# Optimization experiments

Hardware: AMD Instinct MI355X
Metric: run time of the kernel (lower is better)

Reference implementation:

```python
import jax, jax.numpy as jnp
import numpy as np


def setup_inputs() -> dict:
    key = jax.random.key(0)
    ks = jax.random.split(key, 8)
    N, T, U = 8, 512, 64
    E, D, J, V = 512, 512, 512, 500
    s = 0.02
    return {
        "encoder_out": jax.random.normal(ks[0], (N, T, E), jnp.float32),
        "decoder_out": jax.random.normal(ks[1], (N, U, D), jnp.float32),
        "W_enc": jax.random.normal(ks[2], (J, E), jnp.float32) * s,
        "b_enc": jnp.zeros((J,), jnp.float32),
        "W_dec": jax.random.normal(ks[3], (J, D), jnp.float32) * s,
        "b_dec": jnp.zeros((J,), jnp.float32),
        "W_out": jax.random.normal(ks[4], (V, J), jnp.float32) * s,
        "b_out": jnp.zeros((V,), jnp.float32),
    }


def reference(encoder_out, decoder_out, W_enc, b_enc, W_dec, b_dec, W_out, b_out):
    # Project encoder [N,T,E]->[N,T,J] and decoder [N,U,D]->[N,U,J]
    enc = jnp.einsum("nte,je->ntj", encoder_out, W_enc) + b_enc
    dec = jnp.einsum("nud,jd->nuj", decoder_out, W_dec) + b_dec
    # Broadcast add over (T,U), tanh, then vocab projection -> [N,T,U,V]
    activations = jnp.tanh(enc[:, :, None, :] + dec[:, None, :, :])
    logits = jnp.einsum("ntuj,vj->ntuv", activations, W_out) + b_out
    return logits
```

## Files before the change

kernel.cpp:

```cpp
#include <hip/hip_runtime.h>
#include <hip/hip_bf16.h>


typedef __attribute__((ext_vector_type(4))) float f32x4;
typedef __attribute__((ext_vector_type(16))) float f32x16;
typedef __attribute__((ext_vector_type(8))) short s16x8;

static __device__ __forceinline__ unsigned short f2bf(float x) {
    union { float f; unsigned u; } v; v.f = x;
    return (unsigned short)((v.u + 0x7FFFu + ((v.u >> 16) & 1u)) >> 16);
}

static __device__ __forceinline__ float fast_tanh(float x) {
    float e = __expf(2.0f * x);
    float r = __builtin_amdgcn_rcpf(e + 1.0f);
    return __builtin_fmaf(-2.0f, r, 1.0f);
}

static __device__ __forceinline__ unsigned swz64(int r, int c) {
    return (unsigned)(r * 64 + ((c ^ ((r >> 1) & 3)) << 4));
}

__global__ __launch_bounds__(256) void proj_gemm(
    const float* __restrict__ A, const float* __restrict__ W,
    const float* __restrict__ b, float* __restrict__ C)
{
    __shared__ unsigned short As[128 * 64];
    __shared__ unsigned short Bs[128 * 64];
    const int mt = blockIdx.x, jt = blockIdx.y;
    const int tid = threadIdx.x;
    const int lane = tid & 63, wid = tid >> 6;
    const int wm = wid >> 1, wn = wid & 1;

    f32x4 acc[4][4];
    const f32x4 zero = {0.f, 0.f, 0.f, 0.f};
    #pragma unroll
    for (int i = 0; i < 4; ++i)
        #pragma unroll
        for (int j = 0; j < 4; ++j) acc[i][j] = zero;

    const int c8 = (tid & 7) * 8;
    const int rbase = tid >> 3;

    for (int kt = 0; kt < 8; ++kt) {
        __syncthreads();
        #pragma unroll
        for (int p = 0; p < 4; ++p) {
            int r = p * 32 + rbase;
            int byte = (r * 128 + c8 * 2) ^ ((r & 7) << 4);
            {
                const float* s = A + (size_t)(mt * 128 + r) * 512 + kt * 64 + c8;
                f32x4 v0 = *(const f32x4*)s, v1 = *(const f32x4*)(s + 4);
                s16x8 pk;
                pk[0] = (short)f2bf(v0[0]); pk[1] = (short)f2bf(v0[1]);
                pk[2] = (short)f2bf(v0[2]); pk[3] = (short)f2bf(v0[3]);
                pk[4] = (short)f2bf(v1[0]); pk[5] = (short)f2bf(v1[1]);
                pk[6] = (short)f2bf(v1[2]); pk[7] = (short)f2bf(v1[3]);
                *(s16x8*)((char*)As + byte) = pk;
            }
            {
                const float* s = W + (size_t)(jt * 128 + r) * 512 + kt * 64 + c8;
                f32x4 v0 = *(const f32x4*)s, v1 = *(const f32x4*)(s + 4);
                s16x8 pk;
                pk[0] = (short)f2bf(v0[0]); pk[1] = (short)f2bf(v0[1]);
                pk[2] = (short)f2bf(v0[2]); pk[3] = (short)f2bf(v0[3]);
                pk[4] = (short)f2bf(v1[0]); pk[5] = (short)f2bf(v1[1]);
                pk[6] = (short)f2bf(v1[2]); pk[7] = (short)f2bf(v1[3]);
                *(s16x8*)((char*)Bs + byte) = pk;
            }
        }
        __syncthreads();
        #pragma unroll
        for (int kk = 0; kk < 2; ++kk) {
            s16x8 af[4], bfr[4];
            #pragma unroll
            for (int mi = 0; mi < 4; ++mi) {
                int row = wm * 64 + mi * 16 + (lane & 15);
                int byte = (row * 128 + kk * 64 + ((lane >> 4) * 16)) ^ ((row & 7) << 4);
                af[mi] = *(const s16x8*)((const char*)As + byte);
            }
            #pragma unroll
            for (int ni = 0; ni < 4; ++ni) {
                int row = wn * 64 + ni * 16 + (lane & 15);
                int byte = (row * 128 + kk * 64 + ((lane >> 4) * 16)) ^ ((row & 7) << 4);
                bfr[ni] = *(const s16x8*)((const char*)Bs + byte);
            }
            #pragma unroll
            for (int mi = 0; mi < 4; ++mi)
                #pragma unroll
                for (int ni = 0; ni < 4; ++ni)
                    acc[mi][ni] = __builtin_amdgcn_mfma_f32_16x16x32_bf16(
                        af[mi], bfr[ni], acc[mi][ni], 0, 0, 0);
        }
    }

    #pragma unroll
    for (int ni = 0; ni < 4; ++ni) {
        int col = jt * 128 + wn * 64 + ni * 16 + (lane & 15);
        float bias = b[col];
        #pragma unroll
        for (int mi = 0; mi < 4; ++mi) {
            int row0 = mt * 128 + wm * 64 + mi * 16 + ((lane >> 4) << 2);
            #pragma unroll
            for (int j = 0; j < 4; ++j)
                C[(size_t)(row0 + j) * 512 + col] = acc[mi][ni][j] + bias;
        }
    }
}

__global__ __launch_bounds__(256) void conv_wout(
    const float* __restrict__ W, unsigned short* __restrict__ img)
{
    int tid = blockIdx.x * 256 + threadIdx.x;
    int lane = tid & 63;
    int khalf = (tid >> 6) & 1;
    int tile = (tid >> 7) & 15;
    int kt = tid >> 11;
    int v = tile * 32 + (lane & 31);
    int k = kt * 32 + khalf * 16 + (lane >> 5) * 8;
    s16x8 pk = {0, 0, 0, 0, 0, 0, 0, 0};
    if (v < 500) {
        const float* s = W + (size_t)v * 512 + k;
        f32x4 a = *(const f32x4*)s, b = *(const f32x4*)(s + 4);
        pk[0] = (short)f2bf(a[0]); pk[1] = (short)f2bf(a[1]);
        pk[2] = (short)f2bf(a[2]); pk[3] = (short)f2bf(a[3]);
        pk[4] = (short)f2bf(b[0]); pk[5] = (short)f2bf(b[1]);
        pk[6] = (short)f2bf(b[2]); pk[7] = (short)f2bf(b[3]);
    }
    *(s16x8*)(img + (size_t)tid * 8) = pk;
}

__global__ __launch_bounds__(256, 2) void joiner_main(
    const float* __restrict__ enc, const float* __restrict__ dec,
    const unsigned short* __restrict__ Wimg, const float* __restrict__ bout,
    float* __restrict__ out)
{
    __shared__ __align__(16) char raw[66048];
    unsigned short* As0 = (unsigned short*)raw;
    unsigned short* As1 = (unsigned short*)(raw + 4096);
    float* ep = (float*)raw;

    const int bid = blockIdx.x;
    const int tid = threadIdx.x, lane = tid & 63, wn = tid >> 6;
    const int n = bid >> 9, t = bid & 511;

    const float* encN = enc + (size_t)n * (512 * 512);
    const float* decN = dec + (size_t)n * (64 * 512);

    f32x16 acc[2][4];
    #pragma unroll
    for (int i = 0; i < 2; ++i)
        #pragma unroll
        for (int j = 0; j < 4; ++j)
            #pragma unroll
            for (int e = 0; e < 16; ++e) acc[i][j][e] = 0.f;

    const int r = tid >> 2;
    const int c16 = tid & 3;
    const float* erow = encN + (size_t)t * 512 + c16 * 8;
    const float* drow = decN + (size_t)r * 512 + c16 * 8;
    const unsigned abyte = swz64(r, c16);
    const char* wbase = (const char*)Wimg + (size_t)wn * 8192 + (size_t)lane * 16;
    const int lr = lane & 31, kg = lane >> 5;

    f32x4 ee0, ee1, dd0, dd1;
    ee0 = *(const f32x4*)erow;       ee1 = *(const f32x4*)(erow + 4);
    dd0 = *(const f32x4*)drow;       dd1 = *(const f32x4*)(drow + 4);
    {
        s16x8 p;
        p[0] = (short)f2bf(fast_tanh(ee0[0] + dd0[0]));
        p[1] = (short)f2bf(fast_tanh(ee0[1] + dd0[1]));
        p[2] = (short)f2bf(fast_tanh(ee0[2] + dd0[2]));
        p[3] = (short)f2bf(fast_tanh(ee0[3] + dd0[3]));
        p[4] = (short)f2bf(fast_tanh(ee1[0] + dd1[0]));
        p[5] = (short)f2bf(fast_tanh(ee1[1] + dd1[1]));
        p[6] = (short)f2bf(fast_tanh(ee1[2] + dd1[2]));
        p[7] = (short)f2bf(fast_tanh(ee1[3] + dd1[3]));
        *(s16x8*)((char*)As0 + abyte) = p;
        ee0 = *(const f32x4*)(erow + 32);  ee1 = *(const f32x4*)(erow + 36);
        dd0 = *(const f32x4*)(drow + 32);  dd1 = *(const f32x4*)(drow + 36);
    }
    __syncthreads();

    #pragma unroll
    for (int kt = 0; kt < 16; ++kt) {
        const char* Ac = (char*)((kt & 1) ? As1 : As0);
        char* An = (char*)((kt & 1) ? As0 : As1);

        s16x8 bfr[4][2];
        {
            const char* g = wbase + (size_t)kt * 32768;
            #pragma unroll
            for (int ni = 0; ni < 4; ++ni)
                #pragma unroll
                for (int kh = 0; kh < 2; ++kh)
                    bfr[ni][kh] = *(const s16x8*)(g + ni * 2048 + kh * 1024);
        }
        s16x8 af[2][2];
        #pragma unroll
        for (int mi = 0; mi < 2; ++mi)
            #pragma unroll
            for (int kh = 0; kh < 2; ++kh)
                af[mi][kh] = *(const s16x8*)(Ac + swz64(mi * 32 + lr, kh * 2 + kg));
        if (kt < 15) {
            s16x8 p;
            p[0] = (short)f2bf(fast_tanh(ee0[0] + dd0[0]));
            p[1] = (short)f2bf(fast_tanh(ee0[1] + dd0[1]));
            p[2] = (short)f2bf(fast_tanh(ee0[2] + dd0[2]));
            p[3] = (short)f2bf(fast_tanh(ee0[3] + dd0[3]));
            p[4] = (short)f2bf(fast_tanh(ee1[0] + dd1[0]));
            p[5] = (short)f2bf(fast_tanh(ee1[1] + dd1[1]));
            p[6] = (short)f2bf(fast_tanh(ee1[2] + dd1[2]));
            p[7] = (short)f2bf(fast_tanh(ee1[3] + dd1[3]));
            *(s16x8*)(An + abyte) = p;
        }
        if (kt < 14) {
            const float* e_ = erow + (kt + 2) * 32;
            const float* d_ = drow + (kt + 2) * 32;
            ee0 = *(const f32x4*)e_;   ee1 = *(const f32x4*)(e_ + 4);
            dd0 = *(const f32x4*)d_;   dd1 = *(const f32x4*)(d_ + 4);
        }
        #pragma unroll
        for (int kh = 0; kh < 2; ++kh)
            #pragma unroll
            for (int mi = 0; mi < 2; ++mi)
                #pragma unroll
                for (int ni = 0; ni < 4; ++ni)
                    acc[mi][ni] = __builtin_amdgcn_mfma_f32_32x32x16_bf16(
                        bfr[ni][kh], af[mi][kh], acc[mi][ni], 0, 0, 0);
        __syncthreads();
    }

    const int hi4 = (lane >> 5) * 4;
    const size_t slab = (size_t)bid * 64 * 500;
    #pragma unroll
    for (int mi = 0; mi < 2; ++mi) {
        __syncthreads();
        #pragma unroll
        for (int ni = 0; ni < 4; ++ni) {
            int vt = wn * 128 + ni * 32;
            #pragma unroll
            for (int q = 0; q < 4; ++q) {
                int v4 = vt + q * 8 + hi4;
                if (v4 < 500) {
                    f32x4 b = *(const f32x4*)(bout + v4);
                    f32x4 o;
                    o[0] = acc[mi][ni][q * 4 + 0] + b[0];
                    o[1] = acc[mi][ni][q * 4 + 1] + b[1];
                    o[2] = acc[mi][ni][q * 4 + 2] + b[2];
                    o[3] = acc[mi][ni][q * 4 + 3] + b[3];
                    *(f32x4*)(ep + lr * 516 + v4) = o;
                }
            }
        }
        __syncthreads();
        const size_t base = slab + (size_t)mi * (32 * 500);
        #pragma unroll
        for (int i = 0; i < 16; ++i) {
            int idx = i * 256 + tid;
            if (idx < 4000) {
                int rr = idx / 125;
                int vi = (idx - rr * 125) * 4;
                f32x4 ov = *(const f32x4*)(ep + rr * 516 + vi);
                __builtin_nontemporal_store(ov, (f32x4*)(out + base + (size_t)idx * 4));
            }
        }
    }
}

extern "C" void kernel_launch(void* const* d_in, const int* in_sizes, int n_in,
                              void* d_out, int out_size, void* d_ws, size_t ws_size,
                              hipStream_t stream) {
    const float* encoder_out = (const float*)d_in[0];
    const float* decoder_out = (const float*)d_in[1];
    const float* W_enc = (const float*)d_in[2];
    const float* b_enc = (const float*)d_in[3];
    const float* W_dec = (const float*)d_in[4];
    const float* b_dec = (const float*)d_in[5];
    const float* W_out = (const float*)d_in[6];
    const float* b_out = (const float*)d_in[7];
    float* out = (float*)d_out;

    float* enc_p = (float*)d_ws;
    float* dec_p = enc_p + (size_t)8 * 512 * 512;
    unsigned short* wimg = (unsigned short*)(dec_p + (size_t)8 * 64 * 512);

    conv_wout<<<dim3(128), 256, 0, stream>>>(W_out, wimg);
    proj_gemm<<<dim3(32, 4), 256, 0, stream>>>(encoder_out, W_enc, b_enc, enc_p);
    proj_gemm<<<dim3(4, 4), 256, 0, stream>>>(decoder_out, W_dec, b_dec, dec_p);
    joiner_main<<<dim3(4096), 256, 0, stream>>>(enc_p, dec_p, wimg, b_out, out);
}
```

Before: 242.4 us.

## Fuse prep kernels and split joiner tile across eight waves

Merges the W_out conversion and both projection GEMMs into one prep launch to cut launch overhead. The joiner now runs 512 threads with eight waves, each covering 64 vocab columns, which halves accumulators per wave and raises occupancy. Each thread converts four activations instead of eight per k-step, and the epilogue stages 16-row slices through a smaller LDS buffer. The bias is padded to 512 in workspace so the v<500 guard can be dropped, at the cost of an extra memset and copy.

```diff
diff --git a/kernel.cpp b/kernel.cpp
--- a/kernel.cpp
+++ b/kernel.cpp
@@ -4,6 +4,7 @@
 
 typedef __attribute__((ext_vector_type(4))) float f32x4;
 typedef __attribute__((ext_vector_type(16))) float f32x16;
+typedef __attribute__((ext_vector_type(4))) short s16x4;
 typedef __attribute__((ext_vector_type(8))) short s16x8;
 
 static __device__ __forceinline__ unsigned short f2bf(float x) {
@@ -21,13 +22,11 @@
     return (unsigned)(r * 64 + ((c ^ ((r >> 1) & 3)) << 4));
 }
 
-__global__ __launch_bounds__(256) void proj_gemm(
+static __device__ void proj_body(
     const float* __restrict__ A, const float* __restrict__ W,
-    const float* __restrict__ b, float* __restrict__ C)
+    const float* __restrict__ b, float* __restrict__ C,
+    int mt, int jt, unsigned short* As, unsigned short* Bs)
 {
-    __shared__ unsigned short As[128 * 64];
-    __shared__ unsigned short Bs[128 * 64];
-    const int mt = blockIdx.x, jt = blockIdx.y;
     const int tid = threadIdx.x;
     const int lane = tid & 63, wid = tid >> 6;
     const int wm = wid >> 1, wn = wid & 1;
@@ -108,77 +107,82 @@
     }
 }
 
-__global__ __launch_bounds__(256) void conv_wout(
-    const float* __restrict__ W, unsigned short* __restrict__ img)
+__global__ __launch_bounds__(256) void prep(
+    const float* __restrict__ Wout, unsigned short* __restrict__ img,
+    const float* __restrict__ encoder_out, const float* __restrict__ W_enc,
+    const float* __restrict__ b_enc, float* __restrict__ enc_p,
+    const float* __restrict__ decoder_out, const float* __restrict__ W_dec,
+    const float* __restrict__ b_dec, float* __restrict__ dec_p)
 {
-    int tid = blockIdx.x * 256 + threadIdx.x;
-    int lane = tid & 63;
-    int khalf = (tid >> 6) & 1;
-    int tile = (tid >> 7) & 15;
-    int kt = tid >> 11;
-    int v = tile * 32 + (lane & 31);
-    int k = kt * 32 + khalf * 16 + (lane >> 5) * 8;
-    s16x8 pk = {0, 0, 0, 0, 0, 0, 0, 0};
-    if (v < 500) {
-        const float* s = W + (size_t)v * 512 + k;
-        f32x4 a = *(const f32x4*)s, b = *(const f32x4*)(s + 4);
-        pk[0] = (short)f2bf(a[0]); pk[1] = (short)f2bf(a[1]);
-        pk[2] = (short)f2bf(a[2]); pk[3] = (short)f2bf(a[3]);
-        pk[4] = (short)f2bf(b[0]); pk[5] = (short)f2bf(b[1]);
-        pk[6] = (short)f2bf(b[2]); pk[7] = (short)f2bf(b[3]);
-    }
-    *(s16x8*)(img + (size_t)tid * 8) = pk;
-}
-
-__global__ __launch_bounds__(256, 2) void joiner_main(
+    __shared__ unsigned short As[128 * 64];
+    __shared__ unsigned short Bs[128 * 64];
+    const int b = blockIdx.x;
+    if (b < 128) {
+        int tid = b * 256 + threadIdx.x;
+        int lane = tid & 63;
+        int khalf = (tid >> 6) & 1;
+        int tile = (tid >> 7) & 15;
+        int kt = tid >> 11;
+        int v = tile * 32 + (lane & 31);
+        int k = kt * 32 + khalf * 16 + (lane >> 5) * 8;
+        s16x8 pk = {0, 0, 0, 0, 0, 0, 0, 0};
+        if (v < 500) {
+            const float* s = Wout + (size_t)v * 512 + k;
+            f32x4 a = *(const f32x4*)s, c = *(const f32x4*)(s + 4);
+            pk[0] = (short)f2bf(a[0]); pk[1] = (short)f2bf(a[1]);
+            pk[2] = (short)f2bf(a[2]); pk[3] = (short)f2bf(a[3]);
+            pk[4] = (short)f2bf(c[0]); pk[5] = (short)f2bf(c[1]);
+            pk[6] = (short)f2bf(c[2]); pk[7] = (short)f2bf(c[3]);
+        }
+        *(s16x8*)(img + (size_t)tid * 8) = pk;
+    } else if (b < 256) {
+        int q = b - 128;
+        proj_body(encoder_out, W_enc, b_enc, enc_p, q & 31, q >> 5, As, Bs);
+    } else {
+        int q = b - 256;
+        proj_body(decoder_out, W_dec, b_dec, dec_p, q & 3, q >> 2, As, Bs);
+    }
+}
+
+__global__ __launch_bounds__(512, 4) void joiner_main(
     const float* __restrict__ enc, const float* __restrict__ dec,
     const unsigned short* __restrict__ Wimg, const float* __restrict__ bout,
     float* __restrict__ out)
 {
-    __shared__ __align__(16) char raw[66048];
+    __shared__ __align__(16) char raw[8192 + 33024];
     unsigned short* As0 = (unsigned short*)raw;
     unsigned short* As1 = (unsigned short*)(raw + 4096);
-    float* ep = (float*)raw;
+    float* ep = (float*)(raw + 8192);
 
     const int bid = blockIdx.x;
     const int tid = threadIdx.x, lane = tid & 63, wn = tid >> 6;
     const int n = bid >> 9, t = bid & 511;
 
-    const float* encN = enc + (size_t)n * (512 * 512);
-    const float* decN = dec + (size_t)n * (64 * 512);
-
-    f32x16 acc[2][4];
+    f32x16 acc[2][2];
     #pragma unroll
     for (int i = 0; i < 2; ++i)
         #pragma unroll
-        for (int j = 0; j < 4; ++j)
+        for (int j = 0; j < 2; ++j)
             #pragma unroll
             for (int e = 0; e < 16; ++e) acc[i][j][e] = 0.f;
 
-    const int r = tid >> 2;
-    const int c16 = tid & 3;
-    const float* erow = encN + (size_t)t * 512 + c16 * 8;
-    const float* drow = decN + (size_t)r * 512 + c16 * 8;
-    const unsigned abyte = swz64(r, c16);
-    const char* wbase = (const char*)Wimg + (size_t)wn * 8192 + (size_t)lane * 16;
+    const int r = tid >> 3;
+    const int q8 = tid & 7;
+    const float* erow = enc + ((size_t)n * 512 + t) * 512 + q8 * 4;
+    const float* drow = dec + ((size_t)n * 64 + r) * 512 + q8 * 4;
+    const unsigned abyte = swz64(r, q8 >> 1) + (q8 & 1) * 8;
+    const char* wbase = (const char*)Wimg + (size_t)wn * 4096 + (size_t)lane * 16;
     const int lr = lane & 31, kg = lane >> 5;
 
-    f32x4 ee0, ee1, dd0, dd1;
-    ee0 = *(const f32x4*)erow;       ee1 = *(const f32x4*)(erow + 4);
-    dd0 = *(const f32x4*)drow;       dd1 = *(const f32x4*)(drow + 4);
     {
-        s16x8 p;
-        p[0] = (short)f2bf(fast_tanh(ee0[0] + dd0[0]));
-        p[1] = (short)f2bf(fast_tanh(ee0[1] + dd0[1]));
-        p[2] = (short)f2bf(fast_tanh(ee0[2] + dd0[2]));
-        p[3] = (short)f2bf(fast_tanh(ee0[3] + dd0[3]));
-        p[4] = (short)f2bf(fast_tanh(ee1[0] + dd1[0]));
-        p[5] = (short)f2bf(fast_tanh(ee1[1] + dd1[1]));
-        p[6] = (short)f2bf(fast_tanh(ee1[2] + dd1[2]));
-        p[7] = (short)f2bf(fast_tanh(ee1[3] + dd1[3]));
-        *(s16x8*)((char*)As0 + abyte) = p;
-        ee0 = *(const f32x4*)(erow + 32);  ee1 = *(const f32x4*)(erow + 36);
-        dd0 = *(const f32x4*)(drow + 32);  dd1 = *(const f32x4*)(drow + 36);
+        f32x4 e0 = *(const f32x4*)erow;
+        f32x4 d0 = *(const f32x4*)drow;
+        s16x4 p;
+        p[0] = (short)f2bf(fast_tanh(e0[0] + d0[0]));
+        p[1] = (short)f2bf(fast_tanh(e0[1] + d0[1]));
+        p[2] = (short)f2bf(fast_tanh(e0[2] + d0[2]));
+        p[3] = (short)f2bf(fast_tanh(e0[3] + d0[3]));
+        *(s16x4*)((char*)As0 + abyte) = p;
     }
     __syncthreads();
 
@@ -187,11 +191,11 @@
         const char* Ac = (char*)((kt & 1) ? As1 : As0);
         char* An = (char*)((kt & 1) ? As0 : As1);
 
-        s16x8 bfr[4][2];
+        s16x8 bfr[2][2];
         {
             const char* g = wbase + (size_t)kt * 32768;
             #pragma unroll
-            for (int ni = 0; ni < 4; ++ni)
+            for (int ni = 0; ni < 2; ++ni)
                 #pragma unroll
                 for (int kh = 0; kh < 2; ++kh)
                     bfr[ni][kh] = *(const s16x8*)(g + ni * 2048 + kh * 1024);
@@ -203,66 +207,60 @@
             for (int kh = 0; kh < 2; ++kh)
                 af[mi][kh] = *(const s16x8*)(Ac + swz64(mi * 32 + lr, kh * 2 + kg));
         if (kt < 15) {
-            s16x8 p;
-            p[0] = (short)f2bf(fast_tanh(ee0[0] + dd0[0]));
-            p[1] = (short)f2bf(fast_tanh(ee0[1] + dd0[1]));
-            p[2] = (short)f2bf(fast_tanh(ee0[2] + dd0[2]));
-            p[3] = (short)f2bf(fast_tanh(ee0[3] + dd0[3]));
-            p[4] = (short)f2bf(fast_tanh(ee1[0] + dd1[0]));
-            p[5] = (short)f2bf(fast_tanh(ee1[1] + dd1[1]));
-            p[6] = (short)f2bf(fast_tanh(ee1[2] + dd1[2]));
-            p[7] = (short)f2bf(fast_tanh(ee1[3] + dd1[3]));
-            *(s16x8*)(An + abyte) = p;
-        }
-        if (kt < 14) {
-            const float* e_ = erow + (kt + 2) * 32;
-            const float* d_ = drow + (kt + 2) * 32;
-            ee0 = *(const f32x4*)e_;   ee1 = *(const f32x4*)(e_ + 4);
-            dd0 = *(const f32x4*)d_;   dd1 = *(const f32x4*)(d_ + 4);
+            const float* e_ = erow + (kt + 1) * 32;
+            const float* d_ = drow + (kt + 1) * 32;
+            f32x4 e0 = *(const f32x4*)e_;
+            f32x4 d0 = *(const f32x4*)d_;
+            s16x4 p;
+            p[0] = (short)f2bf(fast_tanh(e0[0] + d0[0]));
+            p[1] = (short)f2bf(fast_tanh(e0[1] + d0[1]));
+            p[2] = (short)f2bf(fast_tanh(e0[2] + d0[2]));
+            p[3] = (short)f2bf(fast_tanh(e0[3] + d0[3]));
+            *(s16x4*)(An + abyte) = p;
         }
         #pragma unroll
         for (int kh = 0; kh < 2; ++kh)
             #pragma unroll
             for (int mi = 0; mi < 2; ++mi)
                 #pragma unroll
-                for (int ni = 0; ni < 4; ++ni)
+                for (int ni = 0; ni < 2; ++ni)
                     acc[mi][ni] = __builtin_amdgcn_mfma_f32_32x32x16_bf16(
                         bfr[ni][kh], af[mi][kh], acc[mi][ni], 0, 0, 0);
         __syncthreads();
     }
 
     const int hi4 = (lane >> 5) * 4;
-    const size_t slab = (size_t)bid * 64 * 500;
-    #pragma unroll
-    for (int mi = 0; mi < 2; ++mi) {
-        __syncthreads();
-        #pragma unroll
-        for (int ni = 0; ni < 4; ++ni) {
-            int vt = wn * 128 + ni * 32;
-            #pragma unroll
-            for (int q = 0; q < 4; ++q) {
-                int v4 = vt + q * 8 + hi4;
-                if (v4 < 500) {
+    const int lr16 = lane & 15;
+    #pragma unroll
+    for (int o = 0; o < 4; ++o) {
+        __syncthreads();
+        if (((lane >> 4) & 1) == (o & 1)) {
+            const int mi = o >> 1;
+            #pragma unroll
+            for (int ni = 0; ni < 2; ++ni) {
+                #pragma unroll
+                for (int q = 0; q < 4; ++q) {
+                    int v4 = wn * 64 + ni * 32 + q * 8 + hi4;
                     f32x4 b = *(const f32x4*)(bout + v4);
-                    f32x4 o;
-                    o[0] = acc[mi][ni][q * 4 + 0] + b[0];
-                    o[1] = acc[mi][ni][q * 4 + 1] + b[1];
-                    o[2] = acc[mi][ni][q * 4 + 2] + b[2];
-                    o[3] = acc[mi][ni][q * 4 + 3] + b[3];
-                    *(f32x4*)(ep + lr * 516 + v4) = o;
+                    f32x4 ov;
+                    ov[0] = acc[mi][ni == 0 ? 0 : 1][q * 4 + 0] + b[0];
+                    ov[1] = acc[mi][ni == 0 ? 0 : 1][q * 4 + 1] + b[1];
+                    ov[2] = acc[mi][ni == 0 ? 0 : 1][q * 4 + 2] + b[2];
+                    ov[3] = acc[mi][ni == 0 ? 0 : 1][q * 4 + 3] + b[3];
+                    *(f32x4*)(ep + lr16 * 516 + v4) = ov;
                 }
             }
         }
         __syncthreads();
-        const size_t base = slab + (size_t)mi * (32 * 500);
-        #pragma unroll
-        for (int i = 0; i < 16; ++i) {
-            int idx = i * 256 + tid;
-            if (idx < 4000) {
+        const size_t obase = ((size_t)bid * 64 + o * 16) * 500;
+        #pragma unroll
+        for (int i = 0; i < 4; ++i) {
+            int idx = i * 512 + tid;
+            if (idx < 2000) {
                 int rr = idx / 125;
                 int vi = (idx - rr * 125) * 4;
                 f32x4 ov = *(const f32x4*)(ep + rr * 516 + vi);
-                __builtin_nontemporal_store(ov, (f32x4*)(out + base + (size_t)idx * 4));
+                __builtin_nontemporal_store(ov, (f32x4*)(out + obase + (size_t)idx * 4));
             }
         }
     }
@@ -284,9 +282,12 @@
     float* enc_p = (float*)d_ws;
     float* dec_p = enc_p + (size_t)8 * 512 * 512;
     unsigned short* wimg = (unsigned short*)(dec_p + (size_t)8 * 64 * 512);
-
-    conv_wout<<<dim3(128), 256, 0, stream>>>(W_out, wimg);
-    proj_gemm<<<dim3(32, 4), 256, 0, stream>>>(encoder_out, W_enc, b_enc, enc_p);
-    proj_gemm<<<dim3(4, 4), 256, 0, stream>>>(decoder_out, W_dec, b_dec, dec_p);
-    joiner_main<<<dim3(4096), 256, 0, stream>>>(enc_p, dec_p, wimg, b_out, out);
-}
+    float* bpad = (float*)(wimg + (size_t)8 * 65536 / 2 * 2);
+
+    prep<<<dim3(272), 256, 0, stream>>>(W_out, wimg,
+                                        encoder_out, W_enc, b_enc, enc_p,
+                                        decoder_out, W_dec, b_dec, dec_p);
+    hipMemsetAsync(bpad, 0, 512 * sizeof(float), stream);
+    hipMemcpyAsync(bpad, b_out, 500 * sizeof(float), hipMemcpyDeviceToDevice, stream);
+    joiner_main<<<dim3(4096), 512, 0, stream>>>(enc_p, dec_p, wimg, bpad, out);
+}
```

Result: no change. 239.1 us (-1.4%).
